# Performance work log

Hardware: AMD Instinct MI355X
Metric: run time of the kernel (lower is better)

## Reference

```python
import jax, jax.numpy as jnp
import numpy as np
from jax import lax

B, C, H, W, S = 8, 64, 64, 64, 12
KSIZE = 5


def _conv2d_same(x, w):
    # x: [N, Cin, H, W], w: [Cout, Cin, kh, kw]
    return lax.conv_general_dilated(
        x, w, window_strides=(1, 1), padding='SAME',
        dimension_numbers=('NCHW', 'OIHW', 'NCHW'))


def setup_inputs() -> dict:
    key = jax.random.key(0)
    k0, k1, k2, k3, k4 = jax.random.split(key, 5)
    x = jax.random.normal(k0, (B, C, H, W, S), dtype=jnp.float32)
    w1 = jax.random.normal(k1, (3 * C, C, 1, 1), dtype=jnp.float32) * 0.05
    b1 = jax.random.normal(k2, (3 * C,), dtype=jnp.float32) * 0.05
    w2 = jax.random.normal(k3, (1, 2 * C, KSIZE, KSIZE), dtype=jnp.float32) * 0.05
    b2 = jax.random.normal(k4, (1,), dtype=jnp.float32) * 0.05
    return {'x': x, 'w1': w1, 'b1': b1, 'w2': w2, 'b2': b2}


def reference(x, w1, b1, w2, b2):
    b, c, h, w_, s = x.shape
    # conv1 (1x1) applied per timestep == channel matmul over all timesteps at once
    qkv = jnp.einsum('oc,bchws->bohws', w1[:, :, 0, 0], x) + b1[None, :, None, None, None]
    Q, K, V = jnp.split(qkv, 3, axis=1)  # each [b, c, h, w, s]

    # conv2 on concat(Q_s, K_t) is linear in channels:
    # score(s,t) = convQ(Q[...,s]) + convK(K[...,t]) + bias
    def per_time_conv(z, wsub):
        # z: [b, c, h, w, s] -> fold time into batch -> conv -> [b, h, w, s]
        zb = jnp.moveaxis(z, -1, 1).reshape(b * s, c, h, w_)
        out = _conv2d_same(zb, wsub)  # [b*s, 1, h, w]
        return jnp.moveaxis(out.reshape(b, s, h, w_), 1, -1)  # [b, h, w, s]

    A_q = per_time_conv(Q, w2[:, :c])   # [b, h, w, s] (query index)
    A_k = per_time_conv(K, w2[:, c:])   # [b, h, w, t] (key index)

    # scores: [b, h, w, t, s]
    scores = A_q[:, :, :, None, :] + A_k[:, :, :, :, None] + b2[0]
    attn = jax.nn.softmax(scores, axis=-2)  # softmax over t (keys)

    # weighted sum of V over t -> [b, c, h, w, s]
    V_out = jnp.einsum('bhwts,bchwt->bchws', attn, V)
    return V_out
```

## Files before the change

kernel.cpp:

```cpp
#include <hip/hip_runtime.h>
#include <hip/hip_bf16.h>

#define X_B 8
#define X_C 64
#define X_H 64
#define X_W 64
#define X_S 12

#define WEFF_OFF 0
#define PART_OFF 4096
#define PART_SZ  393216
#define TG_SZ    131072

__global__ __launch_bounds__(256) void k_prep(const float* __restrict__ w1,
                                              const float* __restrict__ w2,
                                              float* __restrict__ weff) {
    int idx = blockIdx.x * 256 + threadIdx.x;
    if (idx >= 64 * 25) return;
    int cp = idx / 25, tap = idx % 25;
    float s = 0.f;
    for (int c = 0; c < 64; ++c)
        s = fmaf(w2[(64 + c) * 25 + tap], w1[(64 + c) * 64 + cp], s);
    weff[cp * 25 + tap] = s;
}

#define PLANE 5444
#define ROWP  272
#define NSTG  3840
__global__ __launch_bounds__(512) void k_conv(const float* __restrict__ x,
                                              const float* __restrict__ weff,
                                              float* __restrict__ part) {
    __shared__ float lds[3 * PLANE];

    const int bid   = blockIdx.x;
    const int b     = bid & 7;
    const int strip = (bid >> 3) & 3;
    const int q     = bid >> 5;

    const int tid = threadIdx.x;
    const int w   = tid & 63;
    const int hq  = tid >> 6;
    const int r0  = strip * 16 - 2;

    if (tid < 240) {
        const int pl  = tid / 80;
        const int rem = tid % 80;
        const int row = rem >> 2;
        const int sl  = rem & 3;
        const int slot = (sl < 2) ? sl : 64 + sl;
        float4 z; z.x = 0.f; z.y = 0.f; z.z = 0.f; z.w = 0.f;
        *(float4*)(lds + pl * PLANE + row * ROWP + slot * 4) = z;
    }

    const float* xb = x + (size_t)(b * 64 + q * 4) * 49152;

    float acc[2][12];
#pragma unroll
    for (int o = 0; o < 2; ++o)
#pragma unroll
        for (int j = 0; j < 12; ++j) acc[o][j] = 0.f;

    float4 pf[8];
#pragma unroll
    for (int k = 0; k < 8; ++k) {
        const int i = tid + k * 512;
        float4 v; v.x = 0.f; v.y = 0.f; v.z = 0.f; v.w = 0.f;
        if (i < NSTG) {
            const int row = i / 192;
            const int j   = i - row * 192;
            const int rg  = r0 + row;
            if ((unsigned)rg < 64u) v = *(const float4*)(xb + rg * 768 + j * 4);
        }
        pf[k] = v;
    }

    for (int ci = 0; ci < 4; ++ci) {
#pragma unroll
        for (int k = 0; k < 8; ++k) {
            const int i = tid + k * 512;
            if (i < NSTG) {
                const int row = i / 192;
                const unsigned j = (unsigned)(i - row * 192);
                const unsigned wj = j / 3u;
                const unsigned tg = j - wj * 3u;
                *(float4*)(lds + tg * PLANE + row * ROWP + (wj + 2) * 4) = pf[k];
            }
        }
        __syncthreads();

        if (ci < 3) {
            const float* xc = xb + (size_t)(ci + 1) * 49152;
#pragma unroll
            for (int k = 0; k < 8; ++k) {
                const int i = tid + k * 512;
                float4 v; v.x = 0.f; v.y = 0.f; v.z = 0.f; v.w = 0.f;
                if (i < NSTG) {
                    const int row = i / 192;
                    const int j   = i - row * 192;
                    const int rg  = r0 + row;
                    if ((unsigned)rg < 64u) v = *(const float4*)(xc + rg * 768 + j * 4);
                }
                pf[k] = v;
            }
        }

        const float* wp = weff + (q * 4 + ci) * 25;
        float wgt[25];
#pragma unroll
        for (int k = 0; k < 25; ++k) wgt[k] = wp[k];

#pragma unroll
        for (int tg = 0; tg < 3; ++tg) {
            const float* lr0 = lds + tg * PLANE + (hq * 2) * ROWP + w * 4;
#pragma unroll
            for (int rr = 0; rr < 6; ++rr) {
                const float* lp = lr0 + rr * ROWP;
#pragma unroll
                for (int dw = 0; dw < 5; ++dw) {
                    float4 v = *(const float4*)(lp + dw * 4);
                    const int olo = (rr - 4 < 0) ? 0 : rr - 4;
                    const int ohi = (rr > 1) ? 1 : rr;
#pragma unroll
                    for (int oo = olo; oo <= ohi; ++oo) {
                        const float g = wgt[(rr - oo) * 5 + dw];
                        acc[oo][tg * 4 + 0] = fmaf(g, v.x, acc[oo][tg * 4 + 0]);
                        acc[oo][tg * 4 + 1] = fmaf(g, v.y, acc[oo][tg * 4 + 1]);
                        acc[oo][tg * 4 + 2] = fmaf(g, v.z, acc[oo][tg * 4 + 2]);
                        acc[oo][tg * 4 + 3] = fmaf(g, v.w, acc[oo][tg * 4 + 3]);
                    }
                }
            }
        }
        __syncthreads();
    }

    float* pb = part + (size_t)q * PART_SZ;
#pragma unroll
    for (int oo = 0; oo < 2; ++oo) {
        const int h = strip * 16 + hq * 2 + oo;
        const int idx = (b * 64 + h) * 64 + w;
#pragma unroll
        for (int tg = 0; tg < 3; ++tg) {
            float4 st;
            st.x = acc[oo][tg * 4 + 0]; st.y = acc[oo][tg * 4 + 1];
            st.z = acc[oo][tg * 4 + 2]; st.w = acc[oo][tg * 4 + 3];
            *(float4*)(pb + (size_t)tg * TG_SZ + (size_t)idx * 4) = st;
        }
    }
}

__global__ __launch_bounds__(256) void k_soft(const float* __restrict__ part,
                                              float* __restrict__ p) {
    const int idx = blockIdx.x * 256 + threadIdx.x;
    if (idx >= 32768) return;
    float v[12];
#pragma unroll
    for (int t = 0; t < 12; ++t) v[t] = 0.f;
#pragma unroll
    for (int qg = 0; qg < 16; ++qg) {
        const float* pp = part + (size_t)qg * PART_SZ;
#pragma unroll
        for (int tg = 0; tg < 3; ++tg) {
            float4 t0 = *(const float4*)(pp + (size_t)tg * TG_SZ + (size_t)idx * 4);
            v[tg * 4 + 0] += t0.x; v[tg * 4 + 1] += t0.y;
            v[tg * 4 + 2] += t0.z; v[tg * 4 + 3] += t0.w;
        }
    }
    float m = v[0];
#pragma unroll
    for (int t = 1; t < 12; ++t) m = fmaxf(m, v[t]);
    float s = 0.f;
#pragma unroll
    for (int t = 0; t < 12; ++t) { v[t] = __expf(v[t] - m); s += v[t]; }
    const float inv = 1.f / s;
#pragma unroll
    for (int t = 0; t < 12; ++t) v[t] *= inv;
    float* op = p + (size_t)idx * 12;
    float4 s0; s0.x = v[0]; s0.y = v[1]; s0.z = v[2];  s0.w = v[3];
    float4 s1; s1.x = v[4]; s1.y = v[5]; s1.z = v[6];  s1.w = v[7];
    float4 s2; s2.x = v[8]; s2.y = v[9]; s2.z = v[10]; s2.w = v[11];
    *(float4*)(op)     = s0;
    *(float4*)(op + 4) = s1;
    *(float4*)(op + 8) = s2;
}

__global__ __launch_bounds__(512) void k_out(const float* __restrict__ x,
                                             const float* __restrict__ w1,
                                             const float* __restrict__ b1,
                                             const float* __restrict__ p,
                                             float* __restrict__ out) {
    __shared__ float lds[64 * 65];

    const int b  = blockIdx.x >> 6;
    const int h  = blockIdx.x & 63;
    const int w  = threadIdx.x & 63;
    const int cg = threadIdx.x >> 6;

    const float* pp = p + (size_t)((b * 64 + h) * 64 + w) * 12;
    float pv[12];
    {
        float4 t0 = *(const float4*)(pp);
        float4 t1 = *(const float4*)(pp + 4);
        float4 t2 = *(const float4*)(pp + 8);
        pv[0] = t0.x; pv[1] = t0.y; pv[2]  = t0.z; pv[3]  = t0.w;
        pv[4] = t1.x; pv[5] = t1.y; pv[6]  = t1.z; pv[7]  = t1.w;
        pv[8] = t2.x; pv[9] = t2.y; pv[10] = t2.z; pv[11] = t2.w;
    }

    const float* xb0 = x + ((size_t)(b * 64 + cg * 8) * 64 + h) * 768 + w * 12;
#pragma unroll
    for (int j = 0; j < 8; ++j) {
        const float* xp = xb0 + (size_t)j * 49152;
        float4 u0 = *(const float4*)(xp);
        float4 u1 = *(const float4*)(xp + 4);
        float4 u2 = *(const float4*)(xp + 8);
        float s = 0.f;
        s = fmaf(pv[0], u0.x, s);  s = fmaf(pv[1], u0.y, s);
        s = fmaf(pv[2], u0.z, s);  s = fmaf(pv[3], u0.w, s);
        s = fmaf(pv[4], u1.x, s);  s = fmaf(pv[5], u1.y, s);
        s = fmaf(pv[6], u1.z, s);  s = fmaf(pv[7], u1.w, s);
        s = fmaf(pv[8], u2.x, s);  s = fmaf(pv[9], u2.y, s);
        s = fmaf(pv[10], u2.z, s); s = fmaf(pv[11], u2.w, s);
        lds[w * 65 + cg * 8 + j] = s;
    }
    __syncthreads();

    const float* w1v = w1 + 128 * 64 + cg * 8 * 64;
    float acc[8];
#pragma unroll
    for (int j = 0; j < 8; ++j) acc[j] = b1[128 + cg * 8 + j];
    for (int c2 = 0; c2 < 64; ++c2) {
        const float xv = lds[w * 65 + c2];
#pragma unroll
        for (int j = 0; j < 8; ++j)
            acc[j] = fmaf(w1v[j * 64 + c2], xv, acc[j]);
    }

#pragma unroll
    for (int j = 0; j < 8; ++j) {
        const int co = cg * 8 + j;
        float4 f; f.x = acc[j]; f.y = acc[j]; f.z = acc[j]; f.w = acc[j];
        float* op = out + ((size_t)(b * 64 + co) * 4096 + h * 64 + w) * 12;
        *(float4*)(op)     = f;
        *(float4*)(op + 4) = f;
        *(float4*)(op + 8) = f;
    }
}

extern "C" void kernel_launch(void* const* d_in, const int* in_sizes, int n_in,
                              void* d_out, int out_size, void* d_ws, size_t ws_size,
                              hipStream_t stream) {
    const float* x  = (const float*)d_in[0];
    const float* w1 = (const float*)d_in[1];
    const float* b1 = (const float*)d_in[2];
    const float* w2 = (const float*)d_in[3];

    float* outp = (float*)d_out;
    float* weff = outp + WEFF_OFF;
    float* part = outp + PART_OFF;
    float* p    = (float*)d_ws;

    hipLaunchKernelGGL(k_prep, dim3(7),    dim3(256), 0, stream, w1, w2, weff);
    hipLaunchKernelGGL(k_conv, dim3(512),  dim3(512), 0, stream, x, weff, part);
    hipLaunchKernelGGL(k_soft, dim3(128),  dim3(256), 0, stream, part, p);
    hipLaunchKernelGGL(k_out,  dim3(512),  dim3(512), 0, stream, x, w1, b1, p, outp);
}
```

Measured before the change: 103.2 us.

## Retile conv kernel to 4x2 register blocks per thread with swizzled LDS

The conv kernel now runs 384 threads per block. Each thread handles one time-group and computes a 4-row by 2-column output tile, so every loaded LDS row is reused across more horizontal and vertical taps (6 float4 loads per row for 10 taps instead of 5 per output). LDS slots are XOR-swizzled to cut bank conflicts from the stride-2 column access. Staging offsets are precomputed once, removing per-iteration divisions. The cost is more registers per thread and fewer threads per block.

```diff
diff --git a/kernel.cpp b/kernel.cpp
--- a/kernel.cpp
+++ b/kernel.cpp
@@ -27,7 +27,7 @@
 #define PLANE 5444
 #define ROWP  272
 #define NSTG  3840
-__global__ __launch_bounds__(512) void k_conv(const float* __restrict__ x,
+__global__ __launch_bounds__(384) void k_conv(const float* __restrict__ x,
                                               const float* __restrict__ weff,
                                               float* __restrict__ part) {
     __shared__ float lds[3 * PLANE];
@@ -38,8 +38,9 @@
     const int q     = bid >> 5;
 
     const int tid = threadIdx.x;
-    const int w   = tid & 63;
-    const int hq  = tid >> 6;
+    const int wp  = tid & 31;
+    const int hq  = (tid >> 5) & 3;
+    const int tg  = tid >> 7;
     const int r0  = strip * 16 - 2;
 
     if (tid < 240) {
@@ -52,81 +53,89 @@
         *(float4*)(lds + pl * PLANE + row * ROWP + slot * 4) = z;
     }
 
+    int ldsoff[10], gloff[10];
+#pragma unroll
+    for (int k = 0; k < 10; ++k) {
+        const int i   = tid + k * 384;
+        const int row = i / 192;
+        const int j   = i - row * 192;
+        const int wj  = j / 3;
+        const int tgw = j - wj * 3;
+        int sl = wj + 2;
+        sl ^= (sl >> 3) & 1;
+        ldsoff[k] = tgw * PLANE + row * ROWP + sl * 4;
+        const int rg = r0 + row;
+        gloff[k] = ((unsigned)rg < 64u) ? (rg * 768 + j * 4) : -1;
+    }
+
+    const float* base[6];
+#pragma unroll
+    for (int k = 0; k < 6; ++k) {
+        int s = 2 * wp + k;
+        s ^= (s >> 3) & 1;
+        base[k] = lds + tg * PLANE + (hq * 4) * ROWP + s * 4;
+    }
+
     const float* xb = x + (size_t)(b * 64 + q * 4) * 49152;
 
-    float acc[2][12];
-#pragma unroll
-    for (int o = 0; o < 2; ++o)
-#pragma unroll
-        for (int j = 0; j < 12; ++j) acc[o][j] = 0.f;
-
-    float4 pf[8];
-#pragma unroll
-    for (int k = 0; k < 8; ++k) {
-        const int i = tid + k * 512;
+    float acc[4][2][4];
+#pragma unroll
+    for (int o = 0; o < 4; ++o)
+#pragma unroll
+        for (int j = 0; j < 2; ++j)
+#pragma unroll
+            for (int t = 0; t < 4; ++t) acc[o][j][t] = 0.f;
+
+    float4 pf[10];
+#pragma unroll
+    for (int k = 0; k < 10; ++k) {
         float4 v; v.x = 0.f; v.y = 0.f; v.z = 0.f; v.w = 0.f;
-        if (i < NSTG) {
-            const int row = i / 192;
-            const int j   = i - row * 192;
-            const int rg  = r0 + row;
-            if ((unsigned)rg < 64u) v = *(const float4*)(xb + rg * 768 + j * 4);
-        }
+        if (gloff[k] >= 0) v = *(const float4*)(xb + gloff[k]);
         pf[k] = v;
     }
 
     for (int ci = 0; ci < 4; ++ci) {
 #pragma unroll
-        for (int k = 0; k < 8; ++k) {
-            const int i = tid + k * 512;
-            if (i < NSTG) {
-                const int row = i / 192;
-                const unsigned j = (unsigned)(i - row * 192);
-                const unsigned wj = j / 3u;
-                const unsigned tg = j - wj * 3u;
-                *(float4*)(lds + tg * PLANE + row * ROWP + (wj + 2) * 4) = pf[k];
-            }
-        }
+        for (int k = 0; k < 10; ++k)
+            *(float4*)(lds + ldsoff[k]) = pf[k];
         __syncthreads();
 
         if (ci < 3) {
             const float* xc = xb + (size_t)(ci + 1) * 49152;
 #pragma unroll
-            for (int k = 0; k < 8; ++k) {
-                const int i = tid + k * 512;
+            for (int k = 0; k < 10; ++k) {
                 float4 v; v.x = 0.f; v.y = 0.f; v.z = 0.f; v.w = 0.f;
-                if (i < NSTG) {
-                    const int row = i / 192;
-                    const int j   = i - row * 192;
-                    const int rg  = r0 + row;
-                    if ((unsigned)rg < 64u) v = *(const float4*)(xc + rg * 768 + j * 4);
-                }
+                if (gloff[k] >= 0) v = *(const float4*)(xc + gloff[k]);
                 pf[k] = v;
             }
         }
 
-        const float* wp = weff + (q * 4 + ci) * 25;
+        const float* wgp = weff + (q * 4 + ci) * 25;
         float wgt[25];
 #pragma unroll
-        for (int k = 0; k < 25; ++k) wgt[k] = wp[k];
-
-#pragma unroll
-        for (int tg = 0; tg < 3; ++tg) {
-            const float* lr0 = lds + tg * PLANE + (hq * 2) * ROWP + w * 4;
-#pragma unroll
-            for (int rr = 0; rr < 6; ++rr) {
-                const float* lp = lr0 + rr * ROWP;
-#pragma unroll
-                for (int dw = 0; dw < 5; ++dw) {
-                    float4 v = *(const float4*)(lp + dw * 4);
-                    const int olo = (rr - 4 < 0) ? 0 : rr - 4;
-                    const int ohi = (rr > 1) ? 1 : rr;
-#pragma unroll
-                    for (int oo = olo; oo <= ohi; ++oo) {
-                        const float g = wgt[(rr - oo) * 5 + dw];
-                        acc[oo][tg * 4 + 0] = fmaf(g, v.x, acc[oo][tg * 4 + 0]);
-                        acc[oo][tg * 4 + 1] = fmaf(g, v.y, acc[oo][tg * 4 + 1]);
-                        acc[oo][tg * 4 + 2] = fmaf(g, v.z, acc[oo][tg * 4 + 2]);
-                        acc[oo][tg * 4 + 3] = fmaf(g, v.w, acc[oo][tg * 4 + 3]);
+        for (int k = 0; k < 25; ++k) wgt[k] = wgp[k];
+
+#pragma unroll
+        for (int rr = 0; rr < 8; ++rr) {
+            float4 v[6];
+#pragma unroll
+            for (int k = 0; k < 6; ++k)
+                v[k] = *(const float4*)(base[k] + rr * ROWP);
+            const int olo = (rr - 4 < 0) ? 0 : rr - 4;
+            const int ohi = (rr > 3) ? 3 : rr;
+#pragma unroll
+            for (int oo = olo; oo <= ohi; ++oo) {
+                const int dh = rr - oo;
+#pragma unroll
+                for (int j = 0; j < 2; ++j) {
+#pragma unroll
+                    for (int dw = 0; dw < 5; ++dw) {
+                        const float g = wgt[dh * 5 + dw];
+                        const float4 vv = v[j + dw];
+                        acc[oo][j][0] = fmaf(g, vv.x, acc[oo][j][0]);
+                        acc[oo][j][1] = fmaf(g, vv.y, acc[oo][j][1]);
+                        acc[oo][j][2] = fmaf(g, vv.z, acc[oo][j][2]);
+                        acc[oo][j][3] = fmaf(g, vv.w, acc[oo][j][3]);
                     }
                 }
             }
@@ -134,17 +143,17 @@
         __syncthreads();
     }
 
-    float* pb = part + (size_t)q * PART_SZ;
-#pragma unroll
-    for (int oo = 0; oo < 2; ++oo) {
-        const int h = strip * 16 + hq * 2 + oo;
-        const int idx = (b * 64 + h) * 64 + w;
-#pragma unroll
-        for (int tg = 0; tg < 3; ++tg) {
+    float* pb = part + (size_t)q * PART_SZ + (size_t)tg * TG_SZ;
+#pragma unroll
+    for (int oo = 0; oo < 4; ++oo) {
+        const int h = strip * 16 + hq * 4 + oo;
+#pragma unroll
+        for (int j = 0; j < 2; ++j) {
+            const int idx = (b * 64 + h) * 64 + 2 * wp + j;
             float4 st;
-            st.x = acc[oo][tg * 4 + 0]; st.y = acc[oo][tg * 4 + 1];
-            st.z = acc[oo][tg * 4 + 2]; st.w = acc[oo][tg * 4 + 3];
-            *(float4*)(pb + (size_t)tg * TG_SZ + (size_t)idx * 4) = st;
+            st.x = acc[oo][j][0]; st.y = acc[oo][j][1];
+            st.z = acc[oo][j][2]; st.w = acc[oo][j][3];
+            *(float4*)(pb + (size_t)idx * 4) = st;
         }
     }
 }
@@ -261,7 +270,7 @@
     float* p    = (float*)d_ws;
 
     hipLaunchKernelGGL(k_prep, dim3(7),    dim3(256), 0, stream, w1, w2, weff);
-    hipLaunchKernelGGL(k_conv, dim3(512),  dim3(512), 0, stream, x, weff, part);
+    hipLaunchKernelGGL(k_conv, dim3(512),  dim3(384), 0, stream, x, weff, part);
     hipLaunchKernelGGL(k_soft, dim3(128),  dim3(256), 0, stream, part, p);
     hipLaunchKernelGGL(k_out,  dim3(512),  dim3(512), 0, stream, x, w1, b1, p, outp);
 }
```

After: 104.9 us. Within noise of the previous version (+1.6%).
